# Optimization experiments

Measured on AMD Instinct MI355X. Metric: run time of the kernel, lower is better.

The kernel has to match this reference:

```python
import jax, jax.numpy as jnp
import numpy as np

B, N, D, P, HMUL, K = 2, 4096, 64, 64, 4, 16
H = D * HMUL  # attn_mlp hidden = 256
EPS = 1e-5


def setup_inputs() -> dict:
    key = jax.random.key(0)
    ks = jax.random.split(key, 18)
    def lin(k, fan_in, shape):
        return (jax.random.normal(k, shape, dtype=jnp.float32) / np.sqrt(fan_in)).astype(jnp.float32)
    return {
        "x": jax.random.normal(ks[0], (B, N, D), dtype=jnp.float32),
        "pos": jax.random.uniform(ks[1], (B, N, 3), dtype=jnp.float32),
        "w_qkv": lin(ks[2], D, (D, 3 * D)), "b_qkv": jnp.zeros((3 * D,), jnp.float32),
        "w_p1": lin(ks[3], 3, (3, P)),     "b_p1": jnp.zeros((P,), jnp.float32),
        "w_p2": lin(ks[4], P, (P, D)),     "b_p2": jnp.zeros((D,), jnp.float32),
        "w_a1": lin(ks[5], D, (D, H)),     "b_a1": jnp.zeros((H,), jnp.float32),
        "w_a2": lin(ks[6], H, (H, D)),     "b_a2": jnp.zeros((D,), jnp.float32),
        "w_fc": lin(ks[7], D, (D, D)),     "b_fc": jnp.zeros((D,), jnp.float32),
        "gamma": jnp.ones((D,), jnp.float32), "beta": jnp.zeros((D,), jnp.float32),
    }


def reference(x, pos, w_qkv, b_qkv, w_p1, b_p1, w_p2, b_p2,
              w_a1, b_a1, w_a2, b_a2, w_fc, b_fc, gamma, beta):
    residual = x
    qkv = x @ w_qkv + b_qkv                      # [B,N,3D]
    q, k, v = jnp.split(qkv, 3, axis=-1)         # each [B,N,D]

    # full O(N^2) pairwise distances for KNN (smallest-k)
    rel = pos[:, :, None, :] - pos[:, None, :, :]       # [B,N,N,3]
    dist = jnp.sqrt(jnp.sum(rel * rel, axis=-1))        # [B,N,N]
    _, idx = jax.lax.top_k(-dist, K)                    # [B,N,K] nearest indices

    # gather neighbors (gather commutes with the pointwise MLPs the torch
    # code applies before its neighbor_select, so math is identical)
    gather = jax.vmap(lambda arr, i: arr[i])            # arr:[N,*], i:[N,K] -> [N,K,*]
    k_nb = gather(k, idx)                               # [B,N,K,D]
    v_nb = gather(v, idx)                               # [B,N,K,D]
    pos_nb = gather(pos, idx)                           # [B,N,K,3]

    qk_map = q[:, :, None, :] - k_nb                    # [B,N,K,D]
    rel_nb = pos[:, :, None, :] - pos_nb                # [B,N,K,3]
    pos_emb = jax.nn.relu(rel_nb @ w_p1 + b_p1) @ w_p2 + b_p2   # [B,N,K,D]

    h = qk_map + pos_emb
    scores = jax.nn.relu(h @ w_a1 + b_a1) @ w_a2 + b_a2          # [B,N,K,D]
    attn = jax.nn.softmax(scores, axis=-2)                       # over K neighbors
    agg = jnp.sum(attn * v_nb, axis=-2)                          # [B,N,D]

    agg = agg @ w_fc + b_fc
    # BatchNorm1d over channel dim D (training-mode batch stats over B and N)
    mean = jnp.mean(agg, axis=(0, 1))
    var = jnp.mean(jnp.square(agg - mean), axis=(0, 1))
    agg = (agg - mean) * jax.lax.rsqrt(var + EPS) * gamma + beta
    return jax.nn.relu(agg) + residual
```

## Files before the change

### kernel.cpp

```cpp
#include <hip/hip_runtime.h>
#include <hip/hip_bf16.h>
#include <math.h>

#define NPTS 4096
#define KNB 16
#define CAP 384
#define QPB 8

typedef __attribute__((ext_vector_type(8))) short bf16x8;
typedef __attribute__((ext_vector_type(4))) float f32x4;
#define MFMA16(a, b, c) __builtin_amdgcn_mfma_f32_16x16x32_bf16(a, b, c, 0, 0, 0)

__device__ __forceinline__ unsigned short f2bf(float f) {
  unsigned int u = __float_as_uint(f);
  unsigned int r = (u + 0x7fffu + ((u >> 16) & 1u)) >> 16;
  return (unsigned short)r;
}
__device__ __forceinline__ float bf2f(unsigned short u) {
  return __uint_as_float((unsigned int)u << 16);
}

__global__ __launch_bounds__(256) void qkv_pack_kernel(
    const float* __restrict__ x, const float* __restrict__ w_qkv,
    const float* __restrict__ b_qkv, float* __restrict__ qkv,
    const float* __restrict__ w_a1, const float* __restrict__ w_a2,
    const float* __restrict__ w_p2, unsigned short* __restrict__ pk1,
    unsigned short* __restrict__ pk2, unsigned short* __restrict__ pkp,
    float* __restrict__ stats) {
  int tid = threadIdx.x, bid = blockIdx.x;

  if (bid == 272) {
    if (tid < 128) stats[tid] = 0.f;
    return;
  }
  if (bid >= 128) {
    int e = (bid - 128) * 256 + tid;
    if (e < 16384) {
      int j = e & 7, lane = (e >> 3) & 63, t = e >> 9;
      int ks = t & 1, nt = t >> 1;
      int k = ks * 32 + ((lane >> 4) << 3) + j, n = nt * 16 + (lane & 15);
      pk1[e] = f2bf(w_a1[k * 256 + n]);
    } else if (e < 32768) {
      int e2 = e - 16384;
      int j = e2 & 7, lane = (e2 >> 3) & 63, t = e2 >> 9;
      int ks = t & 7, nt = t >> 3;
      int k = ks * 32 + ((lane >> 4) << 3) + j, n = nt * 16 + (lane & 15);
      pk2[e2] = f2bf(w_a2[k * 64 + n]);
    } else if (e < 36864) {
      int e3 = e - 32768;
      int j = e3 & 7, lane = (e3 >> 3) & 63, t = e3 >> 9;
      int ks = t & 1, nt = t >> 1;
      int k = ks * 32 + ((lane >> 4) << 3) + j, n = nt * 16 + (lane & 15);
      pkp[e3] = f2bf(w_p2[k * 64 + n]);
    }
    return;
  }

  int lane = tid & 63, w = tid >> 6;
  int m = lane & 15, quad = lane >> 4;
  int r0w = bid * 64 + w * 16;

  const float* xr = x + (size_t)(r0w + m) * 64;
  float xa[8], xb[8];
  *(float4*)&xa[0] = *(const float4*)(xr + quad * 8);
  *(float4*)&xa[4] = *(const float4*)(xr + quad * 8 + 4);
  *(float4*)&xb[0] = *(const float4*)(xr + 32 + quad * 8);
  *(float4*)&xb[4] = *(const float4*)(xr + 32 + quad * 8 + 4);
  bf16x8 a0, a1;
#pragma unroll
  for (int j = 0; j < 8; ++j) {
    a0[j] = (short)f2bf(xa[j]);
    a1[j] = (short)f2bf(xb[j]);
  }

#pragma unroll 4
  for (int nt = 0; nt < 12; ++nt) {
    int n = nt * 16 + m;
    int k0 = quad * 8;
    bf16x8 b0, b1;
#pragma unroll
    for (int j = 0; j < 8; ++j) {
      b0[j] = (short)f2bf(w_qkv[(size_t)(k0 + j) * 192 + n]);
      b1[j] = (short)f2bf(w_qkv[(size_t)(32 + k0 + j) * 192 + n]);
    }
    f32x4 acc = {0.f, 0.f, 0.f, 0.f};
    acc = MFMA16(a0, b0, acc);
    acc = MFMA16(a1, b1, acc);
    float bb = b_qkv[n];
#pragma unroll
    for (int i = 0; i < 4; ++i)
      qkv[(size_t)(r0w + quad * 4 + i) * 192 + n] = acc[i] + bb;
  }
}

__global__ __launch_bounds__(256, 4) void fused_kernel(
    const float* __restrict__ qkv, const float* __restrict__ pos,
    const unsigned short* __restrict__ pk1,
    const unsigned short* __restrict__ pk2,
    const unsigned short* __restrict__ pkp, const float* __restrict__ w_p1,
    const float* __restrict__ b_p1, const float* __restrict__ b_p2,
    const float* __restrict__ b_a1, const float* __restrict__ b_a2,
    const float* __restrict__ w_fc, const float* __restrict__ b_fc,
    float* __restrict__ y, float* __restrict__ stats) {
  __shared__ __align__(16) char smem[38400];
  __shared__ int s_idx[128];

  int tid = threadIdx.x, lane = tid & 63, w = tid >> 6;
  int m = lane & 15, quad = lane >> 4;
  int g0 = blockIdx.x * QPB;
  int b = g0 >> 12;
  const float* posb = pos + (size_t)b * NPTS * 3;

  {
    unsigned int(*cbits)[CAP] = (unsigned int(*)[CAP])smem;
    int(*cidx)[CAP] = (int(*)[CAP])(smem + 12288);
    unsigned long long* wmin = (unsigned long long*)(smem + 25088);
    float* sretry = (float*)(smem + 25120);
    unsigned int* scnt = (unsigned int*)(smem + 25152);
    unsigned long long* sprev = (unsigned long long*)(smem + 25184);
    int* sany = (int*)(smem + 25192);

    float qx[QPB], qy[QPB], qz[QPB];
#pragma unroll
    for (int q = 0; q < QPB; ++q) {
      int i = (g0 + q) & (NPTS - 1);
      qx[q] = posb[i * 3 + 0];
      qy[q] = posb[i * 3 + 1];
      qz[q] = posb[i * 3 + 2];
    }
    if (tid < QPB) scnt[tid] = 0;
    if (tid == 0) sany[0] = 0;
    __syncthreads();

    const float T2 = 0.015625f;
    for (int c = 0; c < NPTS / 256; ++c) {
      int j = c * 256 + tid;
      int j3 = j * 3;
      float px = posb[j3 + 0], py = posb[j3 + 1], pz = posb[j3 + 2];
#pragma unroll
      for (int q = 0; q < QPB; ++q) {
        float dx = qx[q] - px, dy = qy[q] - py, dz = qz[q] - pz;
        float d2 = fmaf(dz, dz, fmaf(dy, dy, dx * dx));
        if (d2 < T2) {
          unsigned int p = atomicAdd(&scnt[q], 1u);
          if (p < CAP) {
            cbits[q][p] = __float_as_uint(d2);
            cidx[q][p] = j;
          }
        }
      }
    }
    __syncthreads();

    if (tid < QPB) {
      int q = tid;
      unsigned int n = scnt[q];
      float nt = 0.f;
      if (n < KNB) nt = 0.0625f;
      else if (n > CAP) nt = 0.00390625f;
      sretry[q] = nt;
      if (nt != 0.f) {
        scnt[q] = 0;
        sany[0] = 1;
      }
    }
    __syncthreads();

    if (sany[0]) {
      float tr[QPB];
#pragma unroll
      for (int q = 0; q < QPB; ++q) tr[q] = sretry[q];
      for (int c = 0; c < NPTS / 256; ++c) {
        int j = c * 256 + tid;
        int j3 = j * 3;
        float px = posb[j3 + 0], py = posb[j3 + 1], pz = posb[j3 + 2];
#pragma unroll
        for (int q = 0; q < QPB; ++q) {
          if (tr[q] != 0.f) {
            float dx = qx[q] - px, dy = qy[q] - py, dz = qz[q] - pz;
            float d2 = fmaf(dz, dz, fmaf(dy, dy, dx * dx));
            if (d2 < tr[q]) {
              unsigned int p = atomicAdd(&scnt[q], 1u);
              if (p < CAP) {
                cbits[q][p] = __float_as_uint(d2);
                cidx[q][p] = j;
              }
            }
          }
        }
      }
      __syncthreads();
    }

    for (int qq = 0; qq < 2; ++qq) {
      int q = w * 2 + qq;
      int L = (int)scnt[q];
      if (L >= KNB && L <= CAP) {
        for (int i = lane; i < L; i += 64) {
          unsigned long long ki = ((unsigned long long)cbits[q][i] << 32) |
                                  (unsigned int)cidx[q][i];
          int rank = 0;
          for (int mm = 0; mm < L; ++mm) {
            unsigned long long km = ((unsigned long long)cbits[q][mm] << 32) |
                                    (unsigned int)cidx[q][mm];
            rank += km < ki;
          }
          if (rank < KNB) s_idx[q * KNB + rank] = cidx[q][i];
        }
      }
    }
    __syncthreads();

    for (int q = 0; q < QPB; ++q) {
      unsigned int n = scnt[q];
      if (n < KNB || n > CAP) {
        unsigned long long prev = 0ull;
        for (int r = 0; r < KNB; ++r) {
          unsigned long long best = ~0ull;
          for (int c = 0; c < NPTS / 256; ++c) {
            int j = c * 256 + tid;
            float dx = qx[q] - posb[j * 3 + 0];
            float dy = qy[q] - posb[j * 3 + 1];
            float dz = qz[q] - posb[j * 3 + 2];
            float d2 = fmaf(dz, dz, fmaf(dy, dy, dx * dx));
            unsigned long long key =
                ((unsigned long long)__float_as_uint(d2) << 32) |
                (unsigned int)j;
            bool ok = (r == 0) || (key > prev);
            best = (ok && key < best) ? key : best;
          }
#pragma unroll
          for (int off = 32; off > 0; off >>= 1) {
            unsigned long long o = __shfl_down(best, off);
            best = best < o ? best : o;
          }
          if (lane == 0) wmin[w] = best;
          __syncthreads();
          if (tid == 0) {
            unsigned long long m0 = wmin[0], m1 = wmin[1];
            unsigned long long m2 = wmin[2], m3 = wmin[3];
            unsigned long long a = m0 < m1 ? m0 : m1;
            unsigned long long d = m2 < m3 ? m2 : m3;
            a = a < d ? a : d;
            s_idx[q * KNB + r] = (int)(unsigned int)a;
            sprev[0] = a;
          }
          __syncthreads();
          prev = sprev[0];
          __syncthreads();
        }
      }
    }
  }
  __syncthreads();

  unsigned short(*region)[72] = (unsigned short(*)[72])smem;
  unsigned short(*s_v)[72] = (unsigned short(*)[72])(smem + 18432);
  float(*s_rel)[32][3] = (float(*)[32][3])(smem + 36864);

  if (lane < 32) {
    int row = 32 * w + lane;
    int p = lane >> 4;
    int g = g0 + 2 * w + p;
    int jb = (b << 12) | s_idx[row];
    s_rel[w][lane][0] = pos[(size_t)g * 3 + 0] - pos[(size_t)jb * 3 + 0];
    s_rel[w][lane][1] = pos[(size_t)g * 3 + 1] - pos[(size_t)jb * 3 + 1];
    s_rel[w][lane][2] = pos[(size_t)g * 3 + 2] - pos[(size_t)jb * 3 + 2];
  }
  for (int rl = 0; rl < 32; ++rl) {
    int row = 32 * w + rl;
    int jb = (b << 12) | s_idx[row];
    s_v[row][lane] = f2bf(qkv[(size_t)jb * 192 + 128 + lane]);
  }

  {
    float w0 = w_p1[lane], w1 = w_p1[64 + lane], w2 = w_p1[128 + lane];
    float bp = b_p1[lane];
    for (int rl = 0; rl < 32; ++rl) {
      int row = 32 * w + rl;
      float rx = s_rel[w][rl][0], ry = s_rel[w][rl][1], rz = s_rel[w][rl][2];
      float e = fmaf(rz, w2, fmaf(ry, w1, fmaf(rx, w0, bp)));
      region[row][lane] = f2bf(fmaxf(e, 0.f));
    }
  }

  {
    bf16x8 ea0[2], ea1[2];
#pragma unroll
    for (int p = 0; p < 2; ++p) {
      ea0[p] = *(const bf16x8*)&region[32 * w + 16 * p + m][quad * 8];
      ea1[p] = *(const bf16x8*)&region[32 * w + 16 * p + m][32 + quad * 8];
    }
#pragma unroll
    for (int nt = 0; nt < 4; ++nt) {
      bf16x8 b0 = *(const bf16x8*)(pkp + ((size_t)(nt * 2 + 0) * 64 + lane) * 8);
      bf16x8 b1 = *(const bf16x8*)(pkp + ((size_t)(nt * 2 + 1) * 64 + lane) * 8);
      int col = nt * 16 + m;
      float bp2 = b_p2[col];
#pragma unroll
      for (int p = 0; p < 2; ++p) {
        f32x4 acc = {0.f, 0.f, 0.f, 0.f};
        acc = MFMA16(ea0[p], b0, acc);
        acc = MFMA16(ea1[p], b1, acc);
        int g = g0 + 2 * w + p;
        float qv = qkv[(size_t)g * 192 + col];
#pragma unroll
        for (int i = 0; i < 4; ++i) {
          int row = 32 * w + 16 * p + quad * 4 + i;
          int jb = (b << 12) | s_idx[row];
          float kv = qkv[(size_t)jb * 192 + 64 + col];
          region[row][col] = f2bf(qv - kv + acc[i] + bp2);
        }
      }
    }
  }

  bf16x8 ha0[2], ha1[2];
#pragma unroll
  for (int p = 0; p < 2; ++p) {
    ha0[p] = *(const bf16x8*)&region[32 * w + 16 * p + m][quad * 8];
    ha1[p] = *(const bf16x8*)&region[32 * w + 16 * p + m][32 + quad * 8];
  }
  f32x4 acc2[2][4];
#pragma unroll
  for (int p = 0; p < 2; ++p)
#pragma unroll
    for (int nt2 = 0; nt2 < 4; ++nt2) acc2[p][nt2] = (f32x4){0.f, 0.f, 0.f, 0.f};

  unsigned short(*s_tc)[72] = (unsigned short(*)[72])(smem + w * 4608);

#pragma unroll
  for (int c = 0; c < 4; ++c) {
#pragma unroll
    for (int ntc = 0; ntc < 4; ++ntc) {
      int nt = 4 * c + ntc;
      bf16x8 b0 = *(const bf16x8*)(pk1 + ((size_t)(nt * 2 + 0) * 64 + lane) * 8);
      bf16x8 b1 = *(const bf16x8*)(pk1 + ((size_t)(nt * 2 + 1) * 64 + lane) * 8);
      int coll = ntc * 16 + m;
      float ba = b_a1[nt * 16 + m];
#pragma unroll
      for (int p = 0; p < 2; ++p) {
        f32x4 t = {0.f, 0.f, 0.f, 0.f};
        t = MFMA16(ha0[p], b0, t);
        t = MFMA16(ha1[p], b1, t);
#pragma unroll
        for (int i = 0; i < 4; ++i)
          s_tc[16 * p + quad * 4 + i][coll] = f2bf(fmaxf(t[i] + ba, 0.f));
      }
    }
#pragma unroll
    for (int sub = 0; sub < 2; ++sub) {
      int ks = c * 2 + sub;
      bf16x8 a[2];
#pragma unroll
      for (int p = 0; p < 2; ++p)
        a[p] = *(const bf16x8*)&s_tc[16 * p + m][sub * 32 + quad * 8];
#pragma unroll
      for (int nt2 = 0; nt2 < 4; ++nt2) {
        bf16x8 bb =
            *(const bf16x8*)(pk2 + ((size_t)(nt2 * 8 + ks) * 64 + lane) * 8);
#pragma unroll
        for (int p = 0; p < 2; ++p) acc2[p][nt2] = MFMA16(a[p], bb, acc2[p][nt2]);
      }
    }
  }

  float ba2[4];
#pragma unroll
  for (int nt2 = 0; nt2 < 4; ++nt2) ba2[nt2] = b_a2[nt2 * 16 + m];
  float aggv[2][4];
#pragma unroll
  for (int p = 0; p < 2; ++p) {
#pragma unroll
    for (int nt2 = 0; nt2 < 4; ++nt2) {
      float sc[4];
#pragma unroll
      for (int i = 0; i < 4; ++i) sc[i] = acc2[p][nt2][i] + ba2[nt2];
      float mx = fmaxf(fmaxf(sc[0], sc[1]), fmaxf(sc[2], sc[3]));
      mx = fmaxf(mx, __shfl_xor(mx, 16));
      mx = fmaxf(mx, __shfl_xor(mx, 32));
      float ex[4], ss = 0.f;
#pragma unroll
      for (int i = 0; i < 4; ++i) {
        ex[i] = exp2f((sc[i] - mx) * 1.4426950408889634f);
        ss += ex[i];
      }
      ss += __shfl_xor(ss, 16);
      ss += __shfl_xor(ss, 32);
      int col = nt2 * 16 + m;
      float nu = 0.f;
#pragma unroll
      for (int i = 0; i < 4; ++i) {
        int row = 32 * w + 16 * p + quad * 4 + i;
        nu = fmaf(ex[i], bf2f(s_v[row][col]), nu);
      }
      nu += __shfl_xor(nu, 16);
      nu += __shfl_xor(nu, 32);
      aggv[p][nt2] = nu / ss;
    }
  }
  __syncthreads();

  float* s_agg = (float*)smem;
  if (quad == 0) {
#pragma unroll
    for (int p = 0; p < 2; ++p)
#pragma unroll
      for (int nt2 = 0; nt2 < 4; ++nt2)
        s_agg[(2 * w + p) * 64 + nt2 * 16 + m] = aggv[p][nt2];
  }
  __syncthreads();

  {
    int c = lane, r = w;
    float acc0 = b_fc[c], acc1 = b_fc[c];
    for (int d = 0; d < 64; ++d) {
      float wv = w_fc[d * 64 + c];
      acc0 = fmaf(s_agg[r * 64 + d], wv, acc0);
      acc1 = fmaf(s_agg[(r + 4) * 64 + d], wv, acc1);
    }
    y[(size_t)(g0 + r) * 64 + c] = acc0;
    y[(size_t)(g0 + r + 4) * 64 + c] = acc1;
    float* s_red = (float*)(smem + 2048);
    float* s_red2 = (float*)(smem + 3072);
    s_red[w * 64 + c] = acc0 + acc1;
    s_red2[w * 64 + c] = acc0 * acc0 + acc1 * acc1;
  }
  __syncthreads();
  if (tid < 64) {
    float* s_red = (float*)(smem + 2048);
    float* s_red2 = (float*)(smem + 3072);
    float s = s_red[tid] + s_red[64 + tid] + s_red[128 + tid] + s_red[192 + tid];
    float s2 =
        s_red2[tid] + s_red2[64 + tid] + s_red2[128 + tid] + s_red2[192 + tid];
    atomicAdd(&stats[tid], s);
    atomicAdd(&stats[64 + tid], s2);
  }
}

__global__ __launch_bounds__(256) void bn_kernel(
    const float* __restrict__ y, const float* __restrict__ x,
    const float* __restrict__ stats, const float* __restrict__ gamma,
    const float* __restrict__ beta, float* __restrict__ out) {
  size_t o = (size_t)blockIdx.x * 256 + threadIdx.x;
  int c = (int)(o & 63);
  const float inv_n = 1.f / 8192.f;
  float mean = stats[c] * inv_n;
  float var = stats[64 + c] * inv_n - mean * mean;
  float inv = rsqrtf(var + 1e-5f);
  float v = (y[o] - mean) * inv * gamma[c] + beta[c];
  out[o] = fmaxf(v, 0.f) + x[o];
}

extern "C" void kernel_launch(void* const* d_in, const int* in_sizes, int n_in,
                              void* d_out, int out_size, void* d_ws,
                              size_t ws_size, hipStream_t stream) {
  const float* x = (const float*)d_in[0];
  const float* pos = (const float*)d_in[1];
  const float* w_qkv = (const float*)d_in[2];
  const float* b_qkv = (const float*)d_in[3];
  const float* w_p1 = (const float*)d_in[4];
  const float* b_p1 = (const float*)d_in[5];
  const float* w_p2 = (const float*)d_in[6];
  const float* b_p2 = (const float*)d_in[7];
  const float* w_a1 = (const float*)d_in[8];
  const float* b_a1 = (const float*)d_in[9];
  const float* w_a2 = (const float*)d_in[10];
  const float* b_a2 = (const float*)d_in[11];
  const float* w_fc = (const float*)d_in[12];
  const float* b_fc = (const float*)d_in[13];
  const float* gamma = (const float*)d_in[14];
  const float* beta = (const float*)d_in[15];

  char* ws = (char*)d_ws;
  float* qkv = (float*)(ws + 0);
  float* y = (float*)(ws + 8912896);
  float* stats = (float*)(ws + 11010048);
  unsigned short* pk1 = (unsigned short*)(ws + 11010560);
  unsigned short* pk2 = (unsigned short*)(ws + 11043328);
  unsigned short* pkp = (unsigned short*)(ws + 11076096);

  hipLaunchKernelGGL(qkv_pack_kernel, dim3(273), dim3(256), 0, stream, x,
                     w_qkv, b_qkv, qkv, w_a1, w_a2, w_p2, pk1, pk2, pkp,
                     stats);
  hipLaunchKernelGGL(fused_kernel, dim3(1024), dim3(256), 0, stream, qkv, pos,
                     pk1, pk2, pkp, w_p1, b_p1, b_p2, b_a1, b_a2, w_fc, b_fc,
                     y, stats);
  hipLaunchKernelGGL(bn_kernel, dim3(2048), dim3(256), 0, stream, y, x, stats,
                     gamma, beta, (float*)d_out);
}
```

Measured before the change: 151.1 us.

## Merge QKV projection and weight packing into fused kernel with atomic-counter handoff

Folds the QKV projection and weight-packing kernel into the main fused kernel. The first 656 blocks do producer work, then each bumps a global counter. Every block runs its KNN search and then spins until the counter reaches the producer count before it reads qkv and the packed weights. This removes a kernel launch boundary and lets the producer work overlap with the KNN phase. The cost is a spin-wait barrier whose correctness depends on all producer blocks being resident or scheduled first, plus a memset launch to clear the counter and the stats.

Result: slower. 302.3 us (+100.1%).

```diff
diff --git a/kernel.cpp b/kernel.cpp
--- a/kernel.cpp
+++ b/kernel.cpp
@@ -6,6 +6,7 @@
 #define KNB 16
 #define CAP 384
 #define QPB 8
+#define PRODS 656
 
 typedef __attribute__((ext_vector_type(8))) short bf16x8;
 typedef __attribute__((ext_vector_type(4))) float f32x4;
@@ -20,96 +21,88 @@
   return __uint_as_float((unsigned int)u << 16);
 }
 
-__global__ __launch_bounds__(256) void qkv_pack_kernel(
+__global__ __launch_bounds__(256, 4) void mono_kernel(
     const float* __restrict__ x, const float* __restrict__ w_qkv,
     const float* __restrict__ b_qkv, float* __restrict__ qkv,
     const float* __restrict__ w_a1, const float* __restrict__ w_a2,
     const float* __restrict__ w_p2, unsigned short* __restrict__ pk1,
     unsigned short* __restrict__ pk2, unsigned short* __restrict__ pkp,
-    float* __restrict__ stats) {
-  int tid = threadIdx.x, bid = blockIdx.x;
-
-  if (bid == 272) {
-    if (tid < 128) stats[tid] = 0.f;
-    return;
-  }
-  if (bid >= 128) {
-    int e = (bid - 128) * 256 + tid;
+    const float* __restrict__ pos, const float* __restrict__ w_p1,
+    const float* __restrict__ b_p1, const float* __restrict__ b_p2,
+    const float* __restrict__ b_a1, const float* __restrict__ b_a2,
+    const float* __restrict__ w_fc, const float* __restrict__ b_fc,
+    float* __restrict__ y, float* __restrict__ stats,
+    unsigned int* __restrict__ cnt) {
+  __shared__ __align__(16) char smem[38400];
+  __shared__ int s_idx[128];
+
+  int tid = threadIdx.x, lane = tid & 63, w = tid >> 6;
+  int m = lane & 15, quad = lane >> 4;
+  int bid = blockIdx.x;
+  int g0 = bid * QPB;
+  int b = g0 >> 12;
+  const float* posb = pos + (size_t)b * NPTS * 3;
+
+  if (bid < 512) {
+    int r0 = bid * 16;
+    const float* xr = x + (size_t)(r0 + m) * 64;
+    float xa[8], xb[8];
+    *(float4*)&xa[0] = *(const float4*)(xr + quad * 8);
+    *(float4*)&xa[4] = *(const float4*)(xr + quad * 8 + 4);
+    *(float4*)&xb[0] = *(const float4*)(xr + 32 + quad * 8);
+    *(float4*)&xb[4] = *(const float4*)(xr + 32 + quad * 8 + 4);
+    bf16x8 a0, a1;
+#pragma unroll
+    for (int j = 0; j < 8; ++j) {
+      a0[j] = (short)f2bf(xa[j]);
+      a1[j] = (short)f2bf(xb[j]);
+    }
+#pragma unroll
+    for (int ntl = 0; ntl < 3; ++ntl) {
+      int nt = w * 3 + ntl;
+      int n = nt * 16 + m;
+      int k0 = quad * 8;
+      bf16x8 b0, b1;
+#pragma unroll
+      for (int j = 0; j < 8; ++j) {
+        b0[j] = (short)f2bf(w_qkv[(size_t)(k0 + j) * 192 + n]);
+        b1[j] = (short)f2bf(w_qkv[(size_t)(32 + k0 + j) * 192 + n]);
+      }
+      f32x4 acc = {0.f, 0.f, 0.f, 0.f};
+      acc = MFMA16(a0, b0, acc);
+      acc = MFMA16(a1, b1, acc);
+      float bb = b_qkv[n];
+#pragma unroll
+      for (int i = 0; i < 4; ++i)
+        qkv[(size_t)(r0 + quad * 4 + i) * 192 + n] = acc[i] + bb;
+    }
+    __threadfence();
+    __syncthreads();
+    if (tid == 0) atomicAdd(cnt, 1u);
+  } else if (bid < PRODS) {
+    int e = (bid - 512) * 256 + tid;
     if (e < 16384) {
-      int j = e & 7, lane = (e >> 3) & 63, t = e >> 9;
+      int j = e & 7, ln = (e >> 3) & 63, t = e >> 9;
       int ks = t & 1, nt = t >> 1;
-      int k = ks * 32 + ((lane >> 4) << 3) + j, n = nt * 16 + (lane & 15);
+      int k = ks * 32 + ((ln >> 4) << 3) + j, n = nt * 16 + (ln & 15);
       pk1[e] = f2bf(w_a1[k * 256 + n]);
     } else if (e < 32768) {
       int e2 = e - 16384;
-      int j = e2 & 7, lane = (e2 >> 3) & 63, t = e2 >> 9;
+      int j = e2 & 7, ln = (e2 >> 3) & 63, t = e2 >> 9;
       int ks = t & 7, nt = t >> 3;
-      int k = ks * 32 + ((lane >> 4) << 3) + j, n = nt * 16 + (lane & 15);
+      int k = ks * 32 + ((ln >> 4) << 3) + j, n = nt * 16 + (ln & 15);
       pk2[e2] = f2bf(w_a2[k * 64 + n]);
     } else if (e < 36864) {
       int e3 = e - 32768;
-      int j = e3 & 7, lane = (e3 >> 3) & 63, t = e3 >> 9;
+      int j = e3 & 7, ln = (e3 >> 3) & 63, t = e3 >> 9;
       int ks = t & 1, nt = t >> 1;
-      int k = ks * 32 + ((lane >> 4) << 3) + j, n = nt * 16 + (lane & 15);
+      int k = ks * 32 + ((ln >> 4) << 3) + j, n = nt * 16 + (ln & 15);
       pkp[e3] = f2bf(w_p2[k * 64 + n]);
     }
-    return;
-  }
-
-  int lane = tid & 63, w = tid >> 6;
-  int m = lane & 15, quad = lane >> 4;
-  int r0w = bid * 64 + w * 16;
-
-  const float* xr = x + (size_t)(r0w + m) * 64;
-  float xa[8], xb[8];
-  *(float4*)&xa[0] = *(const float4*)(xr + quad * 8);
-  *(float4*)&xa[4] = *(const float4*)(xr + quad * 8 + 4);
-  *(float4*)&xb[0] = *(const float4*)(xr + 32 + quad * 8);
-  *(float4*)&xb[4] = *(const float4*)(xr + 32 + quad * 8 + 4);
-  bf16x8 a0, a1;
-#pragma unroll
-  for (int j = 0; j < 8; ++j) {
-    a0[j] = (short)f2bf(xa[j]);
-    a1[j] = (short)f2bf(xb[j]);
-  }
-
-#pragma unroll 4
-  for (int nt = 0; nt < 12; ++nt) {
-    int n = nt * 16 + m;
-    int k0 = quad * 8;
-    bf16x8 b0, b1;
-#pragma unroll
-    for (int j = 0; j < 8; ++j) {
-      b0[j] = (short)f2bf(w_qkv[(size_t)(k0 + j) * 192 + n]);
-      b1[j] = (short)f2bf(w_qkv[(size_t)(32 + k0 + j) * 192 + n]);
-    }
-    f32x4 acc = {0.f, 0.f, 0.f, 0.f};
-    acc = MFMA16(a0, b0, acc);
-    acc = MFMA16(a1, b1, acc);
-    float bb = b_qkv[n];
-#pragma unroll
-    for (int i = 0; i < 4; ++i)
-      qkv[(size_t)(r0w + quad * 4 + i) * 192 + n] = acc[i] + bb;
-  }
-}
-
-__global__ __launch_bounds__(256, 4) void fused_kernel(
-    const float* __restrict__ qkv, const float* __restrict__ pos,
-    const unsigned short* __restrict__ pk1,
-    const unsigned short* __restrict__ pk2,
-    const unsigned short* __restrict__ pkp, const float* __restrict__ w_p1,
-    const float* __restrict__ b_p1, const float* __restrict__ b_p2,
-    const float* __restrict__ b_a1, const float* __restrict__ b_a2,
-    const float* __restrict__ w_fc, const float* __restrict__ b_fc,
-    float* __restrict__ y, float* __restrict__ stats) {
-  __shared__ __align__(16) char smem[38400];
-  __shared__ int s_idx[128];
-
-  int tid = threadIdx.x, lane = tid & 63, w = tid >> 6;
-  int m = lane & 15, quad = lane >> 4;
-  int g0 = blockIdx.x * QPB;
-  int b = g0 >> 12;
-  const float* posb = pos + (size_t)b * NPTS * 3;
+    __threadfence();
+    __syncthreads();
+    if (tid == 0) atomicAdd(cnt, 1u);
+  }
 
   {
     unsigned int(*cbits)[CAP] = (unsigned int(*)[CAP])smem;
@@ -128,6 +121,7 @@
       qy[q] = posb[i * 3 + 1];
       qz[q] = posb[i * 3 + 2];
     }
+    __syncthreads();
     if (tid < QPB) scnt[tid] = 0;
     if (tid == 0) sany[0] = 0;
     __syncthreads();
@@ -252,7 +246,12 @@
       }
     }
   }
+
+  if (tid == 0) {
+    while (atomicAdd(cnt, 0u) < PRODS) __builtin_amdgcn_s_sleep(4);
+  }
   __syncthreads();
+  __threadfence();
 
   unsigned short(*region)[72] = (unsigned short(*)[72])smem;
   unsigned short(*s_v)[72] = (unsigned short(*)[72])(smem + 18432);
@@ -476,16 +475,15 @@
   float* qkv = (float*)(ws + 0);
   float* y = (float*)(ws + 8912896);
   float* stats = (float*)(ws + 11010048);
-  unsigned short* pk1 = (unsigned short*)(ws + 11010560);
-  unsigned short* pk2 = (unsigned short*)(ws + 11043328);
-  unsigned short* pkp = (unsigned short*)(ws + 11076096);
-
-  hipLaunchKernelGGL(qkv_pack_kernel, dim3(273), dim3(256), 0, stream, x,
-                     w_qkv, b_qkv, qkv, w_a1, w_a2, w_p2, pk1, pk2, pkp,
-                     stats);
-  hipLaunchKernelGGL(fused_kernel, dim3(1024), dim3(256), 0, stream, qkv, pos,
-                     pk1, pk2, pkp, w_p1, b_p1, b_p2, b_a1, b_a2, w_fc, b_fc,
-                     y, stats);
+  unsigned int* cnt = (unsigned int*)(ws + 11010560);
+  unsigned short* pk1 = (unsigned short*)(ws + 11010624);
+  unsigned short* pk2 = (unsigned short*)(ws + 11043392);
+  unsigned short* pkp = (unsigned short*)(ws + 11076160);
+
+  hipMemsetAsync(ws + 11010048, 0, 576, stream);
+  hipLaunchKernelGGL(mono_kernel, dim3(1024), dim3(256), 0, stream, x, w_qkv,
+                     b_qkv, qkv, w_a1, w_a2, w_p2, pk1, pk2, pkp, pos, w_p1,
+                     b_p1, b_p2, b_a1, b_a2, w_fc, b_fc, y, stats, cnt);
   hipLaunchKernelGGL(bn_kernel, dim3(2048), dim3(256), 0, stream, y, x, stats,
                      gamma, beta, (float*)d_out);
 }
```
